# Performance work log

Measured on AMD Instinct MI355X. Metric: run time of the kernel, lower is better.

Reference implementation:

```python
import jax, jax.numpy as jnp
import numpy as np

H = 40
W = 40
IN_POINTS = 36


def grid_sample_bilinear_border(img, grid):
    """PyTorch F.grid_sample(mode='bilinear', padding_mode='border', align_corners=False).
    img: (B, C, H, W); grid: (B, P, 2) with (x, y) in [-1, 1]. Returns (B, C, P)."""
    B, C, h, w = img.shape
    # unnormalize (align_corners=False): pix = ((g + 1) * size - 1) / 2
    x = ((grid[..., 0] + 1.0) * w - 1.0) * 0.5
    y = ((grid[..., 1] + 1.0) * h - 1.0) * 0.5
    # border padding: clamp coords into valid range
    x = jnp.clip(x, 0.0, w - 1.0)
    y = jnp.clip(y, 0.0, h - 1.0)
    x0f = jnp.floor(x)
    y0f = jnp.floor(y)
    wx = (x - x0f)[..., None]  # (B, P, 1)
    wy = (y - y0f)[..., None]
    x0 = x0f.astype(jnp.int32)
    y0 = y0f.astype(jnp.int32)
    x1 = jnp.minimum(x0 + 1, w - 1)
    y1 = jnp.minimum(y0 + 1, h - 1)
    imgt = img.transpose(0, 2, 3, 1)  # (B, H, W, C) for channel-last gathers
    b = jnp.arange(B)[:, None]        # (B, 1) broadcasts against (B, P)
    v00 = imgt[b, y0, x0]  # (B, P, C)
    v01 = imgt[b, y0, x1]
    v10 = imgt[b, y1, x0]
    v11 = imgt[b, y1, x1]
    out = (v00 * (1 - wx) * (1 - wy) + v01 * wx * (1 - wy)
           + v10 * (1 - wx) * wy + v11 * wx * wy)
    return out.transpose(0, 2, 1)  # (B, C, P)


def setup_inputs() -> dict:
    key = jax.random.key(0)
    ks = jax.random.split(key, 6)
    bs, c = 128, 256
    content_query = jax.random.normal(ks[0], (bs, c), dtype=jnp.float32)
    reference_point = jax.random.uniform(ks[1], (bs, 2), dtype=jnp.float32)
    feature_map = jax.random.normal(ks[2], (bs, c, H * W), dtype=jnp.float32)
    pos = jax.random.normal(ks[3], (bs, c, H * W), dtype=jnp.float32)
    # small offset weights so sampled points stay mostly in [0,1] (module inits these near zero)
    W_off = jax.random.normal(ks[4], (IN_POINTS * 2, c), dtype=jnp.float32) * 0.02
    b_off = jax.random.uniform(ks[5], (IN_POINTS * 2,), dtype=jnp.float32) - 0.5
    return {"content_query": content_query, "reference_point": reference_point,
            "feature_map": feature_map, "pos": pos, "W_off": W_off, "b_off": b_off}


def reference(content_query, reference_point, feature_map, pos, W_off, b_off):
    bs, c = content_query.shape
    # offset generator: nn.Linear(hidden_dim, in_points*2)
    xy_offsets = (content_query @ W_off.T + b_off).reshape(bs, IN_POINTS, 2)
    sampled_points = xy_offsets + reference_point[:, None, :]  # (bs, P, 2)
    fmap = feature_map.reshape(bs, c, H, W)
    pmap = pos.reshape(bs, c, H, W)
    grid = 2.0 * sampled_points - 1.0
    sampled_features = grid_sample_bilinear_border(fmap, grid)  # (bs, C, P)
    pe = grid_sample_bilinear_border(pmap, grid)                # (bs, C, P)
    return (sampled_features, pe)
```

## Files before the change

kernel.cpp:

```cpp
#include <hip/hip_runtime.h>

#define HH 40
#define WW 40
#define NP 36
#define NC 256
#define NB 128

__global__ __launch_bounds__(128) void points_kernel(
    const float* __restrict__ cq, const float* __restrict__ refp,
    const float* __restrict__ Woff, const float* __restrict__ boff,
    float4* __restrict__ rec_w, int4* __restrict__ rec_i) {
    int b = blockIdx.x;
    __shared__ float4 q[NC / 4];
    __shared__ float offs[2 * NP];
    if (threadIdx.x < NC / 4)
        q[threadIdx.x] = ((const float4*)(cq + b * NC))[threadIdx.x];
    __syncthreads();
    int j = threadIdx.x;
    if (j < 2 * NP) {
        const float4* w = (const float4*)(Woff + j * NC);
        float acc = 0.f;
#pragma unroll
        for (int k = 0; k < NC / 4; ++k) {
            float4 a = q[k], bb = w[k];
            acc = fmaf(a.x, bb.x, acc);
            acc = fmaf(a.y, bb.y, acc);
            acc = fmaf(a.z, bb.z, acc);
            acc = fmaf(a.w, bb.w, acc);
        }
        offs[j] = acc + boff[j];
    }
    __syncthreads();
    int p = threadIdx.x;
    if (p < NP) {
        float sx = offs[2 * p + 0] + refp[b * 2 + 0];
        float sy = offs[2 * p + 1] + refp[b * 2 + 1];
        float x = fminf(fmaxf(sx * (float)WW - 0.5f, 0.f), (float)(WW - 1));
        float y = fminf(fmaxf(sy * (float)HH - 0.5f, 0.f), (float)(HH - 1));
        float x0f = floorf(x), y0f = floorf(y);
        int x0 = (int)x0f, y0 = (int)y0f;
        int x1 = min(x0 + 1, WW - 1), y1 = min(y0 + 1, HH - 1);
        float wx = x - x0f, wy = y - y0f;
        rec_w[b * NP + p] = make_float4((1.f - wx) * (1.f - wy), wx * (1.f - wy),
                                        (1.f - wx) * wy, wx * wy);
        rec_i[b * NP + p] = make_int4(y0 * WW + x0, y0 * WW + x1,
                                      y1 * WW + x0, y1 * WW + x1);
    }
}

__global__ __launch_bounds__(576) void sample_kernel(
    const float* __restrict__ fmap, const float* __restrict__ pmap,
    const float4* __restrict__ rec_w, const int4* __restrict__ rec_i,
    float* __restrict__ out) {
    int t = threadIdx.x;
    int ib = t / NP;
    int p = t - ib * NP;
    int img = blockIdx.x * 16 + ib;
    int b = img >> 8;

    float4 w = rec_w[b * NP + p];
    int4 io = rec_i[b * NP + p];

    long base = (long)img * (HH * WW);
    const float* f = fmap + base;
    const float* g = pmap + base;

    float vf = f[io.x] * w.x + f[io.y] * w.y + f[io.z] * w.z + f[io.w] * w.w;
    float vg = g[io.x] * w.x + g[io.y] * w.y + g[io.z] * w.z + g[io.w] * w.w;

    long oidx = (long)img * NP + p;
    out[oidx] = vf;
    out[(long)NB * NC * NP + oidx] = vg;
}

extern "C" void kernel_launch(void* const* d_in, const int* in_sizes, int n_in,
                              void* d_out, int out_size, void* d_ws, size_t ws_size,
                              hipStream_t stream) {
    const float* cq   = (const float*)d_in[0];
    const float* refp = (const float*)d_in[1];
    const float* fmap = (const float*)d_in[2];
    const float* pmap = (const float*)d_in[3];
    const float* Woff = (const float*)d_in[4];
    const float* boff = (const float*)d_in[5];
    float* out = (float*)d_out;

    float4* rec_w = (float4*)d_ws;
    int4*   rec_i = (int4*)((char*)d_ws + NB * NP * 16);

    points_kernel<<<NB, 128, 0, stream>>>(cq, refp, Woff, boff, rec_w, rec_i);

    sample_kernel<<<(NB * NC) / 16, 576, 0, stream>>>(fmap, pmap, rec_w, rec_i, out);
}
```

Before: 51.30 us.

## Fuse offset computation into sampling kernel and use paired float2 gathers

Merges the point/offset kernel into the sampling kernel, so each block recomputes its batch's offset projection and bilinear weights in shared memory instead of going through a workspace and a second launch. The x0/y0 indices are clamped so that adjacent texels can be fetched with two 8-byte loads per map instead of four scalar loads. This removes a launch and a global round-trip, but repeats the small GEMV in every block (16 times per batch), which adds latency before the gathers.

```diff
diff --git a/kernel.cpp b/kernel.cpp
--- a/kernel.cpp
+++ b/kernel.cpp
@@ -5,68 +5,66 @@
 #define NP 36
 #define NC 256
 #define NB 128
+#define IPB 16
+#define BLK (IPB * NP)
 
-__global__ __launch_bounds__(128) void points_kernel(
+__global__ __launch_bounds__(BLK) void fused_kernel(
     const float* __restrict__ cq, const float* __restrict__ refp,
+    const float* __restrict__ fmap, const float* __restrict__ pmap,
     const float* __restrict__ Woff, const float* __restrict__ boff,
-    float4* __restrict__ rec_w, int4* __restrict__ rec_i) {
-    int b = blockIdx.x;
-    __shared__ float4 q[NC / 4];
+    float* __restrict__ out) {
+    int b = blockIdx.x >> 4;
     __shared__ float offs[2 * NP];
-    if (threadIdx.x < NC / 4)
-        q[threadIdx.x] = ((const float4*)(cq + b * NC))[threadIdx.x];
-    __syncthreads();
+    __shared__ float4 wrec[NP];
+    __shared__ int    irec[NP];
+
     int j = threadIdx.x;
     if (j < 2 * NP) {
-        const float4* w = (const float4*)(Woff + j * NC);
+        const float4* w4 = (const float4*)(Woff + j * NC);
+        const float4* q4 = (const float4*)(cq + b * NC);
         float acc = 0.f;
-#pragma unroll
+#pragma unroll 8
         for (int k = 0; k < NC / 4; ++k) {
-            float4 a = q[k], bb = w[k];
-            acc = fmaf(a.x, bb.x, acc);
-            acc = fmaf(a.y, bb.y, acc);
-            acc = fmaf(a.z, bb.z, acc);
-            acc = fmaf(a.w, bb.w, acc);
+            float4 a = q4[k], ww = w4[k];
+            acc = fmaf(a.x, ww.x, acc);
+            acc = fmaf(a.y, ww.y, acc);
+            acc = fmaf(a.z, ww.z, acc);
+            acc = fmaf(a.w, ww.w, acc);
         }
         offs[j] = acc + boff[j];
     }
     __syncthreads();
-    int p = threadIdx.x;
-    if (p < NP) {
-        float sx = offs[2 * p + 0] + refp[b * 2 + 0];
-        float sy = offs[2 * p + 1] + refp[b * 2 + 1];
+    if (j < NP) {
+        float sx = offs[2 * j + 0] + refp[b * 2 + 0];
+        float sy = offs[2 * j + 1] + refp[b * 2 + 1];
         float x = fminf(fmaxf(sx * (float)WW - 0.5f, 0.f), (float)(WW - 1));
         float y = fminf(fmaxf(sy * (float)HH - 0.5f, 0.f), (float)(HH - 1));
-        float x0f = floorf(x), y0f = floorf(y);
-        int x0 = (int)x0f, y0 = (int)y0f;
-        int x1 = min(x0 + 1, WW - 1), y1 = min(y0 + 1, HH - 1);
-        float wx = x - x0f, wy = y - y0f;
-        rec_w[b * NP + p] = make_float4((1.f - wx) * (1.f - wy), wx * (1.f - wy),
-                                        (1.f - wx) * wy, wx * wy);
-        rec_i[b * NP + p] = make_int4(y0 * WW + x0, y0 * WW + x1,
-                                      y1 * WW + x0, y1 * WW + x1);
+        int x0 = min((int)floorf(x), WW - 2);
+        int y0 = min((int)floorf(y), HH - 2);
+        float wx = x - (float)x0, wy = y - (float)y0;
+        wrec[j] = make_float4((1.f - wx) * (1.f - wy), wx * (1.f - wy),
+                              (1.f - wx) * wy, wx * wy);
+        irec[j] = y0 * WW + x0;
     }
-}
+    __syncthreads();
 
-__global__ __launch_bounds__(576) void sample_kernel(
-    const float* __restrict__ fmap, const float* __restrict__ pmap,
-    const float4* __restrict__ rec_w, const int4* __restrict__ rec_i,
-    float* __restrict__ out) {
-    int t = threadIdx.x;
-    int ib = t / NP;
-    int p = t - ib * NP;
-    int img = blockIdx.x * 16 + ib;
-    int b = img >> 8;
+    int ib = threadIdx.x / NP;
+    int p  = threadIdx.x - ib * NP;
+    int img = blockIdx.x * IPB + ib;
 
-    float4 w = rec_w[b * NP + p];
-    int4 io = rec_i[b * NP + p];
+    float4 w = wrec[p];
+    int i00 = irec[p];
+    const float* f = fmap + (long)img * (HH * WW) + i00;
+    const float* g = pmap + (long)img * (HH * WW) + i00;
 
-    long base = (long)img * (HH * WW);
-    const float* f = fmap + base;
-    const float* g = pmap + base;
+    float2 f0, f1, g0, g1;
+    __builtin_memcpy(&f0, f, 8);
+    __builtin_memcpy(&f1, f + WW, 8);
+    __builtin_memcpy(&g0, g, 8);
+    __builtin_memcpy(&g1, g + WW, 8);
 
-    float vf = f[io.x] * w.x + f[io.y] * w.y + f[io.z] * w.z + f[io.w] * w.w;
-    float vg = g[io.x] * w.x + g[io.y] * w.y + g[io.z] * w.z + g[io.w] * w.w;
+    float vf = f0.x * w.x + f0.y * w.y + f1.x * w.z + f1.y * w.w;
+    float vg = g0.x * w.x + g0.y * w.y + g1.x * w.z + g1.y * w.w;
 
     long oidx = (long)img * NP + p;
     out[oidx] = vf;
@@ -84,10 +82,6 @@
     const float* boff = (const float*)d_in[5];
     float* out = (float*)d_out;
 
-    float4* rec_w = (float4*)d_ws;
-    int4*   rec_i = (int4*)((char*)d_ws + NB * NP * 16);
-
-    points_kernel<<<NB, 128, 0, stream>>>(cq, refp, Woff, boff, rec_w, rec_i);
-
-    sample_kernel<<<(NB * NC) / 16, 576, 0, stream>>>(fmap, pmap, rec_w, rec_i, out);
+    fused_kernel<<<(NB * NC) / IPB, BLK, 0, stream>>>(cq, refp, fmap, pmap,
+                                                      Woff, boff, out);
 }
```

Result: slower. 62.83 us (+22.5%).
